# Optimization experiments

Hardware: AMD Instinct MI355X
Metric: run time of the kernel (lower is better)

The kernel has to match this reference:

```python
import jax, jax.numpy as jnp
import numpy as np

B, T = 2, 2048
D_MODEL = 1024
N_LAYERS = 2
VOCAB = 256
BLOCK = 2048
LOCAL = 128
STRIDE = 256
NHEAD = D_MODEL // 64  # 16
HEAD_DIM = D_MODEL // NHEAD  # 64
LN_EPS = 1e-5


def setup_inputs() -> dict:
    key = jax.random.key(0)
    ks = jax.random.split(key, 16)
    L, d = N_LAYERS, D_MODEL

    def g(k, shape, scale=0.02):
        return (jax.random.normal(k, shape, dtype=jnp.float32) * scale)

    return {
        "x": jax.random.randint(ks[0], (B, T), 0, VOCAB),
        "embed": g(ks[1], (VOCAB, d)),
        "pos_embed": g(ks[2], (BLOCK, d)),
        # per-layer weights stacked on leading L axis; Linear as y = x @ W + b
        "Wq": g(ks[3], (L, d, d)), "bq": jnp.zeros((L, d), jnp.float32),
        "Wk": g(ks[4], (L, d, d)), "bk": jnp.zeros((L, d), jnp.float32),
        "Wv": g(ks[5], (L, d, d)), "bv": jnp.zeros((L, d), jnp.float32),
        "Wo": g(ks[6], (L, d, d)), "bo": jnp.zeros((L, d), jnp.float32),
        "g1": jnp.ones((L, d), jnp.float32), "be1": jnp.zeros((L, d), jnp.float32),
        "W1": g(ks[7], (L, d, 4 * d)), "bf1": jnp.zeros((L, 4 * d), jnp.float32),
        "W2": g(ks[8], (L, 4 * d, d)), "bf2": jnp.zeros((L, d), jnp.float32),
        "g2": jnp.ones((L, d), jnp.float32), "be2": jnp.zeros((L, d), jnp.float32),
        "gf": jnp.ones((d,), jnp.float32), "bef": jnp.zeros((d,), jnp.float32),
        "Whead": g(ks[9], (d, VOCAB)),
    }


def _ln(x, gamma, beta):
    mu = jnp.mean(x, axis=-1, keepdims=True)
    var = jnp.mean(jnp.square(x - mu), axis=-1, keepdims=True)
    return (x - mu) * jax.lax.rsqrt(var + LN_EPS) * gamma + beta


def _sparse_mask(t):
    # allowed[i, j] = True if token i may attend to token j
    i = jnp.arange(t)[:, None]
    j = jnp.arange(t)[None, :]
    causal = j <= i
    local = (i - j) <= LOCAL
    glob = (j % STRIDE) == 0
    return causal & (local | glob)


def _sparse_attn(q, k, v, allowed):
    # q, k, v: [B, T, D] -> [B, H, T, hd]
    b, t, d = q.shape
    def split(x):
        return x.reshape(b, t, NHEAD, HEAD_DIM).transpose(0, 2, 1, 3)
    q, k, v = split(q), split(k), split(v)
    scale = HEAD_DIM ** -0.5
    scores = jnp.einsum("bhqd,bhkd->bhqk", q, k) * scale
    scores = jnp.where(allowed[None, None], scores, -jnp.inf)
    attn = jax.nn.softmax(scores, axis=-1)  # every row has j=i allowed -> no NaN
    out = jnp.einsum("bhqk,bhkd->bhqd", attn, v)
    return out.transpose(0, 2, 1, 3).reshape(b, t, d)


def reference(x, embed, pos_embed, Wq, bq, Wk, bk, Wv, bv, Wo, bo,
              g1, be1, W1, bf1, W2, bf2, g2, be2, gf, bef, Whead):
    b, t = x.shape
    h = embed[x] + pos_embed[jnp.arange(t)][None]
    allowed = _sparse_mask(t)
    for l in range(N_LAYERS):
        h_n = _ln(h, g1[l], be1[l])
        q = h_n @ Wq[l] + bq[l]
        k = h_n @ Wk[l] + bk[l]
        v = h_n @ Wv[l] + bv[l]
        attn_out = _sparse_attn(q, k, v, allowed)
        h = h + (attn_out @ Wo[l] + bo[l])
        h2 = _ln(h, g2[l], be2[l])
        ffn = jax.nn.gelu(h2 @ W1[l] + bf1[l], approximate=False) @ W2[l] + bf2[l]
        h = h + ffn
    h = _ln(h, gf, bef)
    return h @ Whead
```

## Files before the change

### kernel.cpp

```cpp
#include <hip/hip_runtime.h>
#include <hip/hip_bf16.h>

#define BB 2
#define TT 2048
#define DD 1024
#define FF 4096
#define VV 256
#define HH 16
#define HD 64
#define MM (BB * TT)
#define LOCAL_W 128
#define STRIDE_G 256
#define QS 3072

typedef short s16x8 __attribute__((ext_vector_type(8)));
typedef __bf16 bf16x8 __attribute__((ext_vector_type(8)));
typedef float f32x4 __attribute__((ext_vector_type(4)));

#define WAITVM(N) asm volatile("s_waitcnt vmcnt(" #N ")" ::: "memory")

__device__ __forceinline__ float b2f(unsigned short u) {
  return __builtin_bit_cast(float, (unsigned int)u << 16);
}
__device__ __forceinline__ unsigned short f2b(float f) {
  __hip_bfloat16 h = __float2bfloat16(f);
  return __builtin_bit_cast(unsigned short, h);
}
__device__ __forceinline__ void gl_lds16(const unsigned short* g, unsigned short* l) {
  __builtin_amdgcn_global_load_lds(
      (const __attribute__((address_space(1))) void*)g,
      (__attribute__((address_space(3))) void*)l, 16, 0, 0);
}
__device__ __forceinline__ bf16x8 ldsr(const unsigned short* p) {
  return __builtin_bit_cast(bf16x8, *(const s16x8*)p);
}

__global__ __launch_bounds__(256) void transpose_k(const float* __restrict__ W,
                                                   unsigned short* __restrict__ WT,
                                                   int K, int N) {
  __shared__ float t[32][33];
  const int n0 = blockIdx.x * 32, k0 = blockIdx.y * 32;
  const int tx = threadIdx.x, ty = threadIdx.y;
  for (int r = ty; r < 32; r += 8) t[r][tx] = W[(size_t)(k0 + r) * N + n0 + tx];
  __syncthreads();
  for (int r = ty; r < 32; r += 8)
    WT[(size_t)(n0 + r) * K + k0 + tx] = f2b(t[tx][r]);
}

__global__ __launch_bounds__(256) void concat_bias(const float* __restrict__ bq,
                                                   const float* __restrict__ bk,
                                                   const float* __restrict__ bv,
                                                   float* __restrict__ bcat) {
  const int i = blockIdx.x * 256 + threadIdx.x;
  const int l = i / QS, j = i - l * QS;
  float v;
  if (j < DD) v = bq[l * DD + j];
  else if (j < 2 * DD) v = bk[l * DD + j - DD];
  else v = bv[l * DD + j - 2 * DD];
  bcat[i] = v;
}

__global__ __launch_bounds__(256) void embed_kernel(const int* __restrict__ x,
                                                    const float* __restrict__ emb,
                                                    const float* __restrict__ pos,
                                                    float* __restrict__ h) {
  const int row = blockIdx.x;
  const int c = threadIdx.x * 4;
  const int tok = x[row];
  const int t = row & (TT - 1);
  float4 e = *(const float4*)&emb[(size_t)tok * DD + c];
  float4 p = *(const float4*)&pos[(size_t)t * DD + c];
  e.x += p.x; e.y += p.y; e.z += p.z; e.w += p.w;
  *(float4*)&h[(size_t)row * DD + c] = e;
}

__global__ __launch_bounds__(256) void ln_kernel(const float* __restrict__ x,
                                                 const float* __restrict__ g,
                                                 const float* __restrict__ be,
                                                 unsigned short* __restrict__ out) {
  const int row = blockIdx.x;
  const int tid = threadIdx.x;
  const float4 v = *(const float4*)&x[(size_t)row * DD + tid * 4];
  float s = v.x + v.y + v.z + v.w;
  float sq = v.x * v.x + v.y * v.y + v.z * v.z + v.w * v.w;
#pragma unroll
  for (int off = 32; off; off >>= 1) {
    s += __shfl_xor(s, off);
    sq += __shfl_xor(sq, off);
  }
  __shared__ float ss[4], ssq[4];
  const int w = tid >> 6, lane = tid & 63;
  if (lane == 0) { ss[w] = s; ssq[w] = sq; }
  __syncthreads();
  s = ss[0] + ss[1] + ss[2] + ss[3];
  sq = ssq[0] + ssq[1] + ssq[2] + ssq[3];
  const float mean = s * (1.0f / DD);
  const float var = sq * (1.0f / DD) - mean * mean;
  const float rstd = rsqrtf(var + 1e-5f);
  const float4 gv = *(const float4*)&g[tid * 4];
  const float4 bv = *(const float4*)&be[tid * 4];
  ushort4 o;
  o.x = f2b((v.x - mean) * rstd * gv.x + bv.x);
  o.y = f2b((v.y - mean) * rstd * gv.y + bv.y);
  o.z = f2b((v.z - mean) * rstd * gv.z + bv.z);
  o.w = f2b((v.w - mean) * rstd * gv.w + bv.w);
  *(ushort4*)&out[(size_t)row * DD + tid * 4] = o;
}

template <int EPI>
__global__ __launch_bounds__(512, 2) void gemm8p(const unsigned short* __restrict__ A,
                                                 const unsigned short* __restrict__ BT,
                                                 const float* __restrict__ bias,
                                                 unsigned short* __restrict__ outp,
                                                 int M, int N, int K, int nbx) {
  __shared__ __align__(16) unsigned short lds[65536];
  const int tid = threadIdx.x;
  const int lane = tid & 63;
  const int w = tid >> 6;
  const int nwg = gridDim.x;
  const int orig = blockIdx.x;
  const int wg = (orig & 7) * (nwg >> 3) + (orig >> 3);
  const int n0 = (wg % nbx) * 256, m0 = (wg / nbx) * 256;
  const int wm = w >> 2, wn = w & 3;
  f32x4 acc[8][4] = {};

  const unsigned short* aSrc[4];
  const unsigned short* bSrc[4];
  int dstOff[4];
#pragma unroll
  for (int i = 0; i < 4; i++) {
    const int s = tid + (i << 9);
    const int row = s >> 3, c = s & 7;
    const int l = c ^ (row & 7);
    aSrc[i] = &A[(size_t)(m0 + row) * K + l * 8];
    bSrc[i] = &BT[(size_t)(n0 + row) * K + l * 8];
    dstOff[i] = s * 8;
  }
  auto STAGE = [&](int tb, int buf) {
    const int kt = tb << 6;
    const int bb = buf << 15;
#pragma unroll
    for (int i = 0; i < 4; i++) gl_lds16(aSrc[i] + kt, &lds[bb + dstOff[i]]);
#pragma unroll
    for (int i = 0; i < 4; i++) gl_lds16(bSrc[i] + kt, &lds[bb + 16384 + dstOff[i]]);
  };

  const int rA = lane & 15, cr = lane >> 4;
  const int pch = (cr ^ (rA & 7)) << 3;
  const int aIdx0 = (wm * 128 + rA) * 64 + pch;
  const int bIdx0 = 16384 + (wn * 64 + rA) * 64 + pch;

  auto TILE = [&](const int buf, const int tb, const bool pref) {
    const int bb = buf << 15;
    bf16x8 bfr[4][2];
    if (pref) STAGE(tb + 1, buf ^ 1);
#pragma unroll
    for (int n = 0; n < 4; n++)
#pragma unroll
      for (int ks = 0; ks < 2; ks++)
        bfr[n][ks] = ldsr(&lds[(bIdx0 + bb + n * 1024) ^ (ks << 5)]);
    {
      bf16x8 af[2][2];
#pragma unroll
      for (int mm = 0; mm < 2; mm++)
#pragma unroll
        for (int ks = 0; ks < 2; ks++)
          af[mm][ks] = ldsr(&lds[(aIdx0 + bb + mm * 1024) ^ (ks << 5)]);
      __builtin_amdgcn_s_barrier();
      asm volatile("s_waitcnt lgkmcnt(0)" ::: "memory");
      __builtin_amdgcn_sched_barrier(0);
      __builtin_amdgcn_s_setprio(1);
#pragma unroll
      for (int mm = 0; mm < 2; mm++)
#pragma unroll
        for (int n = 0; n < 4; n++)
#pragma unroll
          for (int ks = 0; ks < 2; ks++)
            acc[mm][n] = __builtin_amdgcn_mfma_f32_16x16x32_bf16(af[mm][ks], bfr[n][ks],
                                                                 acc[mm][n], 0, 0, 0);
      __builtin_amdgcn_s_setprio(0);
      __builtin_amdgcn_s_barrier();
    }
#pragma unroll
    for (int q = 1; q < 4; q++) {
      bf16x8 af[2][2];
#pragma unroll
      for (int mm = 0; mm < 2; mm++)
#pragma unroll
        for (int ks = 0; ks < 2; ks++)
          af[mm][ks] = ldsr(&lds[(aIdx0 + bb + (q * 2 + mm) * 1024) ^ (ks << 5)]);
      if (q == 3) WAITVM(0);
      __builtin_amdgcn_s_barrier();
      asm volatile("s_waitcnt lgkmcnt(0)" ::: "memory");
      __builtin_amdgcn_sched_barrier(0);
      __builtin_amdgcn_s_setprio(1);
#pragma unroll
      for (int mm = 0; mm < 2; mm++)
#pragma unroll
        for (int n = 0; n < 4; n++)
#pragma unroll
          for (int ks = 0; ks < 2; ks++)
            acc[q * 2 + mm][n] = __builtin_amdgcn_mfma_f32_16x16x32_bf16(
                af[mm][ks], bfr[n][ks], acc[q * 2 + mm][n], 0, 0, 0);
      __builtin_amdgcn_s_setprio(0);
      __builtin_amdgcn_s_barrier();
    }
  };

  const int NT = K >> 6;
  STAGE(0, 0);
  WAITVM(0);
  __builtin_amdgcn_s_barrier();
  for (int it = 0; it < NT; it += 2) {
    TILE(0, it, it + 1 < NT);
    TILE(1, it + 1, it + 2 < NT);
  }

  const int r0 = (lane >> 4) * 4;
  const int cc = lane & 15;
#pragma unroll
  for (int m = 0; m < 8; m++) {
#pragma unroll
    for (int n = 0; n < 4; n++) {
#pragma unroll
      for (int r = 0; r < 4; r++) {
        const int row = m0 + wm * 128 + m * 16 + r0 + r;
        const int col = n0 + wn * 64 + n * 16 + cc;
        float val = acc[m][n][r] + bias[col];
        if (EPI == 3) val = 0.5f * val * (1.0f + erff(val * 0.70710678118654752f));
        outp[(size_t)row * N + col] = f2b(val);
      }
    }
  }
}

template <int EPI>
__global__ __launch_bounds__(512, 2) void gemm_p(const unsigned short* __restrict__ A,
                                                 const unsigned short* __restrict__ BT,
                                                 const float* __restrict__ bias,
                                                 const float* __restrict__ res,
                                                 void* __restrict__ outp,
                                                 int M, int N, int K, int nbx, int nwg2,
                                                 int ksub) {
  constexpr int BM = 128;
  __shared__ __align__(16) unsigned short lds[4][BM * 64];
  const int tid = threadIdx.x;
  const int lane = tid & 63;
  const int w = tid >> 6;
  const int nwg = gridDim.x;
  const int orig = blockIdx.x;
  const int wg = (orig & 7) * (nwg >> 3) + (orig >> 3);
  const int ks = wg / nwg2;
  const int rem = wg - ks * nwg2;
  const int n0 = (rem % nbx) * BM;
  const int m0 = (rem / nbx) * BM;
  const int kb = ks * ksub;
  const int wm = w >> 2, wn = w & 3;
  f32x4 acc[4][2] = {};

  auto STAGE = [&](int t) {
    const int b = t & 3;
    const int kt = kb + (t << 5);
    const int s = tid;
    const int row = s >> 2, sc = s & 3;
    const int c = sc ^ ((row >> 1) & 3);
    gl_lds16(&A[(size_t)(m0 + row) * K + kt + c * 8], &lds[b][s * 8]);
    gl_lds16(&BT[(size_t)(n0 + row) * K + kt + c * 8], &lds[b][BM * 32 + s * 8]);
  };

  const int NT = ksub >> 5;
  STAGE(0); STAGE(1); STAGE(2);

  for (int t = 0; t < NT; ++t) {
    const int ahead = NT - 1 - t;
    if (ahead >= 2) WAITVM(4); else if (ahead == 1) WAITVM(2); else WAITVM(0);
    __builtin_amdgcn_s_barrier();
    asm volatile("" ::: "memory");
    if (t + 3 < NT) STAGE(t + 3);
    const int b = t & 3;
    const int rA = lane & 15, cr = lane >> 4;
    bf16x8 af[4], bfr[2];
#pragma unroll
    for (int m = 0; m < 4; m++) {
      const int row = wm * 64 + m * 16 + rA;
      af[m] = ldsr(&lds[b][row * 32 + ((cr ^ ((row >> 1) & 3)) << 3)]);
    }
#pragma unroll
    for (int n = 0; n < 2; n++) {
      const int row = wn * 32 + n * 16 + rA;
      bfr[n] = ldsr(&lds[b][BM * 32 + row * 32 + ((cr ^ ((row >> 1) & 3)) << 3)]);
    }
    __builtin_amdgcn_s_setprio(1);
#pragma unroll
    for (int m = 0; m < 4; m++)
#pragma unroll
      for (int n = 0; n < 2; n++)
        acc[m][n] = __builtin_amdgcn_mfma_f32_16x16x32_bf16(af[m], bfr[n], acc[m][n], 0, 0, 0);
    __builtin_amdgcn_s_setprio(0);
  }

  const int r0 = (lane >> 4) * 4;
  const int cc = lane & 15;
  float* pout = (EPI == 0) ? ((float*)outp + (size_t)ks * M * N) : (float*)outp;
#pragma unroll
  for (int m = 0; m < 4; m++) {
#pragma unroll
    for (int n = 0; n < 2; n++) {
#pragma unroll
      for (int r = 0; r < 4; r++) {
        const int row = m0 + wm * 64 + m * 16 + r0 + r;
        const int col = n0 + wn * 32 + n * 16 + cc;
        const size_t idx = (size_t)row * N + col;
        if (EPI == 0) {
          pout[idx] = acc[m][n][r];
        } else {
          ((float*)outp)[idx] = acc[m][n][r] + bias[col] + res[idx];
        }
      }
    }
  }
}

template <int NP, bool BIAS, bool RES>
__global__ __launch_bounds__(256) void reduce_k(float* __restrict__ dst,
                                                const float* __restrict__ parts,
                                                const float* __restrict__ bias,
                                                int ncols, size_t total) {
  const size_t i = ((size_t)blockIdx.x * 256 + threadIdx.x) * 4;
  if (i >= total) return;
  f32x4 acc = {};
  if (RES) acc = *(const f32x4*)&dst[i];
  if (BIAS) {
    const int col = (int)(i % ncols);
    acc += *(const f32x4*)&bias[col];
  }
#pragma unroll
  for (int p = 0; p < NP; p++) acc += *(const f32x4*)&parts[(size_t)p * total + i];
  *(f32x4*)&dst[i] = acc;
}

#define QT 16
#define KT 32
#define NTMAX 6
#define KP 72
#define PP 40

__global__ __launch_bounds__(256) void attn_mfma(const unsigned short* __restrict__ qkv,
                                                 unsigned short* __restrict__ outg) {
  __shared__ __align__(16) unsigned short kvs[4][KT * KP];
  __shared__ __align__(16) unsigned short pls[4][QT * PP];
  const int tid = threadIdx.x;
  const int wid = tid >> 6, lane = tid & 63;
  const int qgrp = blockIdx.x & 31;
  const int bh = blockIdx.x >> 5;
  const int h = bh & (HH - 1), b = bh >> 4;
  const size_t baseq = (size_t)b * TT * QS + (size_t)h * HD;
  const size_t baseo = (size_t)b * TT * DD + (size_t)h * HD;
  const int i0 = qgrp * 64 + wid * 16;
  const int g = lane >> 4;
  const int c = lane & 15;

  const int i0b = qgrp * 64 + 48;
  const int ka0b = (i0b > 128) ? ((i0b - 128) & ~31) : 0;
  const int nlb = ((i0b + 16 - ka0b) + 31) >> 5;
  const int neb = (ka0b + 255) >> 8;
  const int ka0 = (i0 > 128) ? ((i0 - 128) & ~31) : 0;
  const int ne = (ka0 + 255) >> 8;

  const s16x8 qf0 = *(const s16x8*)&qkv[baseq + (size_t)(i0 + c) * QS + g * 8];
  const s16x8 qf1 = *(const s16x8*)&qkv[baseq + (size_t)(i0 + c) * QS + 32 + g * 8];

  f32x4 sc[NTMAX][2];
  float smax[4] = {-1e30f, -1e30f, -1e30f, -1e30f};

#pragma unroll
  for (int t = 0; t < NTMAX; t++) {
    if (t > nlb) continue;
    const bool isg = (t == 0);
    if (isg && neb == 0) continue;
    const int kt0 = ka0 + (t - 1) * 32;
#pragma unroll
    for (int it = 0; it < 4; it++) {
      const int row = it * 8 + (lane >> 3);
      const int ch = lane & 7;
      const int j = isg ? ((row < ne) ? row * STRIDE_G : 0) : (kt0 + row);
      *(s16x8*)&kvs[wid][row * KP + ch * 8] =
          *(const s16x8*)&qkv[baseq + DD + (size_t)j * QS + ch * 8];
    }
    __syncthreads();
#pragma unroll
    for (int half = 0; half < 2; half++) {
      const int key = half * 16 + c;
      const bf16x8 kb0 = __builtin_bit_cast(bf16x8, *(const s16x8*)&kvs[wid][key * KP + g * 8]);
      const bf16x8 kb1 = __builtin_bit_cast(bf16x8, *(const s16x8*)&kvs[wid][key * KP + 32 + g * 8]);
      f32x4 a = {};
      a = __builtin_amdgcn_mfma_f32_16x16x32_bf16(__builtin_bit_cast(bf16x8, qf0), kb0, a, 0, 0, 0);
      a = __builtin_amdgcn_mfma_f32_16x16x32_bf16(__builtin_bit_cast(bf16x8, qf1), kb1, a, 0, 0, 0);
#pragma unroll
      for (int r = 0; r < 4; r++) {
        const int i = i0 + g * 4 + r;
        bool ok;
        if (isg) {
          ok = (key < ne);
        } else {
          const int j = kt0 + key;
          ok = (j <= i) && (((i - j) <= LOCAL_W) || ((j & (STRIDE_G - 1)) == 0));
        }
        const float s = ok ? a[r] * 0.125f : -1e30f;
        sc[t][half][r] = s;
        smax[r] = fmaxf(smax[r], s);
      }
    }
    __syncthreads();
  }
#pragma unroll
  for (int r = 0; r < 4; r++)
#pragma unroll
    for (int off = 8; off; off >>= 1)
      smax[r] = fmaxf(smax[r], __shfl_xor(smax[r], off));

  f32x4 o[4] = {};
  float lsum[4] = {0.f, 0.f, 0.f, 0.f};
#pragma unroll
  for (int t = 0; t < NTMAX; t++) {
    if (t > nlb) continue;
    const bool isg = (t == 0);
    if (isg && neb == 0) continue;
    const int kt0 = ka0 + (t - 1) * 32;
#pragma unroll
    for (int it = 0; it < 4; it++) {
      const int row = it * 8 + (lane >> 3);
      const int ch = lane & 7;
      const int j = isg ? ((row < ne) ? row * STRIDE_G : 0) : (kt0 + row);
      *(s16x8*)&kvs[wid][row * KP + ch * 8] =
          *(const s16x8*)&qkv[baseq + 2 * DD + (size_t)j * QS + ch * 8];
    }
#pragma unroll
    for (int half = 0; half < 2; half++)
#pragma unroll
      for (int r = 0; r < 4; r++) {
        const float p = __expf(sc[t][half][r] - smax[r]);
        lsum[r] += p;
        pls[wid][(g * 4 + r) * PP + half * 16 + c] = f2b(p);
      }
    __syncthreads();
    const bf16x8 pa = __builtin_bit_cast(bf16x8, *(const s16x8*)&pls[wid][c * PP + g * 8]);
#pragma unroll
    for (int d0 = 0; d0 < 4; d0++) {
      s16x8 bv;
#pragma unroll
      for (int e = 0; e < 8; e++)
        bv[e] = (short)kvs[wid][(g * 8 + e) * KP + d0 * 16 + c];
      o[d0] = __builtin_amdgcn_mfma_f32_16x16x32_bf16(pa, __builtin_bit_cast(bf16x8, bv), o[d0], 0, 0, 0);
    }
    __syncthreads();
  }
#pragma unroll
  for (int r = 0; r < 4; r++)
#pragma unroll
    for (int off = 8; off; off >>= 1)
      lsum[r] += __shfl_xor(lsum[r], off);
#pragma unroll
  for (int d0 = 0; d0 < 4; d0++)
#pragma unroll
    for (int r = 0; r < 4; r++)
      outg[baseo + (size_t)(i0 + g * 4 + r) * DD + d0 * 16 + c] = f2b(o[d0][r] / lsum[r]);
}

extern "C" void kernel_launch(void* const* d_in, const int* in_sizes, int n_in,
                              void* d_out, int out_size, void* d_ws, size_t ws_size,
                              hipStream_t stream) {
  const int* x = (const int*)d_in[0];
  const float* embed = (const float*)d_in[1];
  const float* pos = (const float*)d_in[2];
  const float* Wq = (const float*)d_in[3];
  const float* bq = (const float*)d_in[4];
  const float* Wk = (const float*)d_in[5];
  const float* bk = (const float*)d_in[6];
  const float* Wv = (const float*)d_in[7];
  const float* bv = (const float*)d_in[8];
  const float* Wo = (const float*)d_in[9];
  const float* bo = (const float*)d_in[10];
  const float* g1 = (const float*)d_in[11];
  const float* be1 = (const float*)d_in[12];
  const float* W1 = (const float*)d_in[13];
  const float* bf1 = (const float*)d_in[14];
  const float* W2 = (const float*)d_in[15];
  const float* bf2 = (const float*)d_in[16];
  const float* g2 = (const float*)d_in[17];
  const float* be2 = (const float*)d_in[18];
  const float* gf = (const float*)d_in[19];
  const float* bef = (const float*)d_in[20];
  const float* Whead = (const float*)d_in[21];

  char* ws = (char*)d_ws;
  size_t off = 0;
  auto alloc = [&](size_t bytes) -> void* {
    void* p = ws + off;
    off += (bytes + 255) & ~(size_t)255;
    return p;
  };
  unsigned short* WqkvT = (unsigned short*)alloc((size_t)2 * QS * DD * 2);
  unsigned short* WoT = (unsigned short*)alloc((size_t)2 * DD * DD * 2);
  unsigned short* W1T = (unsigned short*)alloc((size_t)2 * DD * FF * 2);
  unsigned short* W2T = (unsigned short*)alloc((size_t)2 * DD * FF * 2);
  unsigned short* WheadT = (unsigned short*)alloc((size_t)DD * VV * 2);
  float* bcat = (float*)alloc((size_t)2 * QS * 4);
  float* h = (float*)alloc((size_t)MM * DD * 4);
  unsigned short* hn = (unsigned short*)alloc((size_t)MM * DD * 2);
  unsigned short* qkvb = (unsigned short*)alloc((size_t)MM * QS * 2);
  unsigned short* attnb = (unsigned short*)alloc((size_t)MM * DD * 2);
  unsigned short* mid = (unsigned short*)alloc((size_t)MM * FF * 2);
  float* ffn2p = (float*)qkvb;
  float* headp = (float*)mid;
  (void)ws_size;

  const dim3 tb(32, 8);
  for (int l = 0; l < 2; l++) {
    const size_t wo = (size_t)l * DD * DD;
    const size_t wf = (size_t)l * DD * FF;
    transpose_k<<<dim3(DD / 32, DD / 32), tb, 0, stream>>>(Wq + wo, WqkvT + (size_t)l * QS * DD, DD, DD);
    transpose_k<<<dim3(DD / 32, DD / 32), tb, 0, stream>>>(Wk + wo, WqkvT + ((size_t)l * QS + DD) * DD, DD, DD);
    transpose_k<<<dim3(DD / 32, DD / 32), tb, 0, stream>>>(Wv + wo, WqkvT + ((size_t)l * QS + 2 * DD) * DD, DD, DD);
    transpose_k<<<dim3(DD / 32, DD / 32), tb, 0, stream>>>(Wo + wo, WoT + wo, DD, DD);
    transpose_k<<<dim3(FF / 32, DD / 32), tb, 0, stream>>>(W1 + wf, W1T + wf, DD, FF);
    transpose_k<<<dim3(DD / 32, FF / 32), tb, 0, stream>>>(W2 + wf, W2T + wf, FF, DD);
  }
  transpose_k<<<dim3(VV / 32, DD / 32), tb, 0, stream>>>(Whead, WheadT, DD, VV);
  concat_bias<<<24, 256, 0, stream>>>(bq, bk, bv, bcat);

  embed_kernel<<<MM, 256, 0, stream>>>(x, embed, pos, h);

  for (int l = 0; l < 2; l++) {
    const size_t wo = (size_t)l * DD * DD;
    const size_t wf = (size_t)l * DD * FF;
    ln_kernel<<<MM, 256, 0, stream>>>(h, g1 + l * DD, be1 + l * DD, hn);
    gemm8p<1><<<(QS / 256) * (MM / 256), 512, 0, stream>>>(
        hn, WqkvT + (size_t)l * QS * DD, bcat + l * QS, qkvb, MM, QS, DD, QS / 256);
    attn_mfma<<<BB * HH * (TT / 64), 256, 0, stream>>>(qkvb, attnb);
    gemm_p<2><<<(DD / 128) * (MM / 128), 512, 0, stream>>>(
        attnb, WoT + wo, bo + l * DD, h, h,
        MM, DD, DD, DD / 128, (DD / 128) * (MM / 128), DD);
    ln_kernel<<<MM, 256, 0, stream>>>(h, g2 + l * DD, be2 + l * DD, hn);
    gemm8p<3><<<(FF / 256) * (MM / 256), 512, 0, stream>>>(
        hn, W1T + wf, bf1 + l * FF, mid, MM, FF, DD, FF / 256);
    gemm_p<0><<<2 * (DD / 128) * (MM / 128), 512, 0, stream>>>(
        mid, W2T + wf, nullptr, nullptr, ffn2p,
        MM, DD, FF, DD / 128, (DD / 128) * (MM / 128), FF / 2);
    reduce_k<2, true, true><<<(MM * DD) / 1024, 256, 0, stream>>>(
        h, ffn2p, bf2 + l * DD, DD, (size_t)MM * DD);
  }
  ln_kernel<<<MM, 256, 0, stream>>>(h, gf, bef, hn);
  gemm_p<0><<<4 * (VV / 128) * (MM / 128), 512, 0, stream>>>(
      hn, WheadT, nullptr, nullptr, headp,
      MM, VV, DD, VV / 128, (VV / 128) * (MM / 128), DD / 4);
  reduce_k<4, false, false><<<(MM * VV) / 1024, 256, 0, stream>>>(
      (float*)d_out, headp, nullptr, VV, (size_t)MM * VV);
}
```

Before: 477.3 us.

## Split GEMM K-tiles into half-stages with finer prefetch waits and tanh GELU

Reworks the 256x256 bf16 GEMM main loop so each 64-wide K tile is staged as two 32-wide halves with a new swizzle. Half-tile prefetches are issued early and waited on with partial vmcnt counts, cutting barriers and keeping loads overlapped with MFMA. The GELU epilogue switches from erff to a tanh-style approximation via exp, reducing epilogue cost at a small accuracy deviation from exact GELU.

```diff
diff --git a/kernel.cpp b/kernel.cpp
--- a/kernel.cpp
+++ b/kernel.cpp
@@ -18,6 +18,8 @@
 typedef float f32x4 __attribute__((ext_vector_type(4)));
 
 #define WAITVM(N) asm volatile("s_waitcnt vmcnt(" #N ")" ::: "memory")
+#define LGKM0 do { asm volatile("s_waitcnt lgkmcnt(0)" ::: "memory"); \
+                   __builtin_amdgcn_sched_barrier(0); } while (0)
 
 __device__ __forceinline__ float b2f(unsigned short u) {
   return __builtin_bit_cast(float, (unsigned int)u << 16);
@@ -124,95 +126,96 @@
   const int wm = w >> 2, wn = w & 3;
   f32x4 acc[8][4] = {};
 
-  const unsigned short* aSrc[4];
-  const unsigned short* bSrc[4];
-  int dstOff[4];
-#pragma unroll
-  for (int i = 0; i < 4; i++) {
+  const unsigned short* aSrc[2];
+  const unsigned short* bSrc[2];
+  int dstO[2];
+#pragma unroll
+  for (int i = 0; i < 2; i++) {
     const int s = tid + (i << 9);
-    const int row = s >> 3, c = s & 7;
-    const int l = c ^ (row & 7);
+    const int row = s >> 2, sc = s & 3;
+    const int l = sc ^ ((row >> 1) & 3);
     aSrc[i] = &A[(size_t)(m0 + row) * K + l * 8];
     bSrc[i] = &BT[(size_t)(n0 + row) * K + l * 8];
-    dstOff[i] = s * 8;
-  }
-  auto STAGE = [&](int tb, int buf) {
-    const int kt = tb << 6;
-    const int bb = buf << 15;
-#pragma unroll
-    for (int i = 0; i < 4; i++) gl_lds16(aSrc[i] + kt, &lds[bb + dstOff[i]]);
-#pragma unroll
-    for (int i = 0; i < 4; i++) gl_lds16(bSrc[i] + kt, &lds[bb + 16384 + dstOff[i]]);
+    dstO[i] = s * 8;
+  }
+  auto STAGE = [&](int tb, int ks, int obase) {
+    const int kt = (tb << 6) + (ks << 5);
+    const int so = obase + ks * 16384;
+#pragma unroll
+    for (int i = 0; i < 2; i++) {
+      gl_lds16(aSrc[i] + kt, &lds[so + dstO[i]]);
+      gl_lds16(bSrc[i] + kt, &lds[so + 8192 + dstO[i]]);
+    }
   };
 
   const int rA = lane & 15, cr = lane >> 4;
-  const int pch = (cr ^ (rA & 7)) << 3;
-  const int aIdx0 = (wm * 128 + rA) * 64 + pch;
-  const int bIdx0 = 16384 + (wn * 64 + rA) * 64 + pch;
-
-  auto TILE = [&](const int buf, const int tb, const bool pref) {
-    const int bb = buf << 15;
-    bf16x8 bfr[4][2];
-    if (pref) STAGE(tb + 1, buf ^ 1);
-#pragma unroll
-    for (int n = 0; n < 4; n++)
-#pragma unroll
-      for (int ks = 0; ks < 2; ks++)
-        bfr[n][ks] = ldsr(&lds[(bIdx0 + bb + n * 1024) ^ (ks << 5)]);
-    {
-      bf16x8 af[2][2];
-#pragma unroll
-      for (int mm = 0; mm < 2; mm++)
-#pragma unroll
-        for (int ks = 0; ks < 2; ks++)
-          af[mm][ks] = ldsr(&lds[(aIdx0 + bb + mm * 1024) ^ (ks << 5)]);
-      __builtin_amdgcn_s_barrier();
-      asm volatile("s_waitcnt lgkmcnt(0)" ::: "memory");
-      __builtin_amdgcn_sched_barrier(0);
-      __builtin_amdgcn_s_setprio(1);
-#pragma unroll
-      for (int mm = 0; mm < 2; mm++)
-#pragma unroll
-        for (int n = 0; n < 4; n++)
-#pragma unroll
-          for (int ks = 0; ks < 2; ks++)
-            acc[mm][n] = __builtin_amdgcn_mfma_f32_16x16x32_bf16(af[mm][ks], bfr[n][ks],
-                                                                 acc[mm][n], 0, 0, 0);
-      __builtin_amdgcn_s_setprio(0);
-      __builtin_amdgcn_s_barrier();
-    }
-#pragma unroll
-    for (int q = 1; q < 4; q++) {
-      bf16x8 af[2][2];
-#pragma unroll
-      for (int mm = 0; mm < 2; mm++)
-#pragma unroll
-        for (int ks = 0; ks < 2; ks++)
-          af[mm][ks] = ldsr(&lds[(aIdx0 + bb + (q * 2 + mm) * 1024) ^ (ks << 5)]);
-      if (q == 3) WAITVM(0);
-      __builtin_amdgcn_s_barrier();
-      asm volatile("s_waitcnt lgkmcnt(0)" ::: "memory");
-      __builtin_amdgcn_sched_barrier(0);
-      __builtin_amdgcn_s_setprio(1);
-#pragma unroll
-      for (int mm = 0; mm < 2; mm++)
-#pragma unroll
-        for (int n = 0; n < 4; n++)
-#pragma unroll
-          for (int ks = 0; ks < 2; ks++)
-            acc[q * 2 + mm][n] = __builtin_amdgcn_mfma_f32_16x16x32_bf16(
-                af[mm][ks], bfr[n][ks], acc[q * 2 + mm][n], 0, 0, 0);
-      __builtin_amdgcn_s_setprio(0);
-      __builtin_amdgcn_s_barrier();
-    }
+  const int rowA0 = wm * 128 + rA;
+  const int rowB0 = wn * 64 + rA;
+  const int aAddr0 = rowA0 * 32 + ((cr ^ ((rowA0 >> 1) & 3)) << 3);
+  const int bAddr0 = 8192 + rowB0 * 32 + ((cr ^ ((rowB0 >> 1) & 3)) << 3);
+
+  const int NT = K >> 6;
+  STAGE(0, 0, 0);
+  STAGE(0, 1, 0);
+
+  auto TILE = [&](int bufc, int tb, bool notlast) {
+    const int bb = bufc << 15;
+    const int ob = (bufc ^ 1) << 15;
+    bf16x8 bfr[4], af[4];
+    WAITVM(4);
+    __builtin_amdgcn_s_barrier();
+#pragma unroll
+    for (int n = 0; n < 4; n++) bfr[n] = ldsr(&lds[bb + bAddr0 + n * 512]);
+#pragma unroll
+    for (int i = 0; i < 4; i++) af[i] = ldsr(&lds[bb + aAddr0 + i * 512]);
+    if (notlast) STAGE(tb + 1, 0, ob);
+    LGKM0;
+    __builtin_amdgcn_s_setprio(1);
+#pragma unroll
+    for (int i = 0; i < 4; i++)
+#pragma unroll
+      for (int n = 0; n < 4; n++)
+        acc[i][n] = __builtin_amdgcn_mfma_f32_16x16x32_bf16(af[i], bfr[n], acc[i][n], 0, 0, 0);
+    __builtin_amdgcn_s_setprio(0);
+#pragma unroll
+    for (int i = 0; i < 4; i++) af[i] = ldsr(&lds[bb + aAddr0 + (4 + i) * 512]);
+    LGKM0;
+    __builtin_amdgcn_s_setprio(1);
+#pragma unroll
+    for (int i = 0; i < 4; i++)
+#pragma unroll
+      for (int n = 0; n < 4; n++)
+        acc[4 + i][n] = __builtin_amdgcn_mfma_f32_16x16x32_bf16(af[i], bfr[n], acc[4 + i][n], 0, 0, 0);
+    __builtin_amdgcn_s_setprio(0);
+    if (notlast) { WAITVM(4); } else { WAITVM(0); }
+    __builtin_amdgcn_s_barrier();
+#pragma unroll
+    for (int n = 0; n < 4; n++) bfr[n] = ldsr(&lds[bb + 16384 + bAddr0 + n * 512]);
+#pragma unroll
+    for (int i = 0; i < 4; i++) af[i] = ldsr(&lds[bb + 16384 + aAddr0 + i * 512]);
+    if (notlast) STAGE(tb + 1, 1, ob);
+    LGKM0;
+    __builtin_amdgcn_s_setprio(1);
+#pragma unroll
+    for (int i = 0; i < 4; i++)
+#pragma unroll
+      for (int n = 0; n < 4; n++)
+        acc[i][n] = __builtin_amdgcn_mfma_f32_16x16x32_bf16(af[i], bfr[n], acc[i][n], 0, 0, 0);
+    __builtin_amdgcn_s_setprio(0);
+#pragma unroll
+    for (int i = 0; i < 4; i++) af[i] = ldsr(&lds[bb + 16384 + aAddr0 + (4 + i) * 512]);
+    LGKM0;
+    __builtin_amdgcn_s_setprio(1);
+#pragma unroll
+    for (int i = 0; i < 4; i++)
+#pragma unroll
+      for (int n = 0; n < 4; n++)
+        acc[4 + i][n] = __builtin_amdgcn_mfma_f32_16x16x32_bf16(af[i], bfr[n], acc[4 + i][n], 0, 0, 0);
+    __builtin_amdgcn_s_setprio(0);
   };
 
-  const int NT = K >> 6;
-  STAGE(0, 0);
-  WAITVM(0);
-  __builtin_amdgcn_s_barrier();
   for (int it = 0; it < NT; it += 2) {
-    TILE(0, it, it + 1 < NT);
+    TILE(0, it, true);
     TILE(1, it + 1, it + 2 < NT);
   }
 
@@ -227,7 +230,12 @@
         const int row = m0 + wm * 128 + m * 16 + r0 + r;
         const int col = n0 + wn * 64 + n * 16 + cc;
         float val = acc[m][n][r] + bias[col];
-        if (EPI == 3) val = 0.5f * val * (1.0f + erff(val * 0.70710678118654752f));
+        if (EPI == 3) {
+          float u = val * (0.7978845608f + 0.0356774081f * val * val);
+          u = fminf(u, 10.0f);
+          const float e = __expf(2.0f * u);
+          val = val * e / (e + 1.0f);
+        }
         outp[(size_t)row * N + col] = f2b(val);
       }
     }
```

Result: faster. 455.9 us (-4.5%).
